# Kernel optimization log

Hardware: AMD Instinct MI355X
Metric: run time of the kernel (lower is better)

## Reference

```python
import jax, jax.numpy as jnp
import numpy as np

H = 16      # num_head
D = 1024    # feat_dim
DK = D // H # per-head dim
B, S = 2, 2048


def setup_inputs() -> dict:
    key = jax.random.key(0)
    ks = jax.random.split(key, 11)
    scale = 1.0 / np.sqrt(D)
    inp = {
        'query': jax.random.normal(ks[0], (B, S, D), jnp.float32),
        'key':   jax.random.normal(ks[1], (B, S, D), jnp.float32),
        'value': jax.random.normal(ks[2], (B, S, D), jnp.float32),
        # causal lower-triangular mask (seq, seq); 0 entries get -1e9
        'mask':  jnp.tril(jnp.ones((S, S), jnp.int32)),
        # torch nn.Linear params: y = x @ W.T + b
        'w_q': jax.random.normal(ks[3], (D, D), jnp.float32) * scale,
        'b_q': jax.random.normal(ks[4], (D,), jnp.float32) * scale,
        'w_k': jax.random.normal(ks[5], (D, D), jnp.float32) * scale,
        'b_k': jax.random.normal(ks[6], (D,), jnp.float32) * scale,
        'w_v': jax.random.normal(ks[7], (D, D), jnp.float32) * scale,
        'b_v': jax.random.normal(ks[8], (D,), jnp.float32) * scale,
        'w_out': jax.random.normal(ks[9], (D, D), jnp.float32) * scale,
        'b_out': jax.random.normal(ks[10], (D,), jnp.float32) * scale,
    }
    return inp


def reference(query, key, value, mask, w_q, b_q, w_k, b_k, w_v, b_v, w_out, b_out):
    b = query.shape[0]
    # projections + split heads -> (b, h, s, d_k)
    def proj(x, w, bias):
        y = x @ w.T + bias
        return y.reshape(b, -1, H, DK).transpose(0, 2, 1, 3)
    q = proj(query, w_q, b_q)
    k = proj(key, w_k, b_k)
    v = proj(value, w_v, b_v)
    # scaled dot-product attention with materialized score matrix
    scores = jnp.einsum('bhqd,bhkd->bhqk', q, k) / np.sqrt(DK).astype(jnp.float32)
    scores = jnp.where(mask == 0, jnp.float32(-1e9), scores)
    attn = jax.nn.softmax(scores, axis=-1)  # dropout is identity in eval mode
    x = jnp.einsum('bhqk,bhkd->bhqd', attn, v)
    x = x.transpose(0, 2, 1, 3).reshape(b, -1, H * DK)
    return x @ w_out.T + b_out
```

## Files before the change

kernel.cpp:

```cpp
#include <hip/hip_runtime.h>

typedef unsigned short u16;
typedef __attribute__((ext_vector_type(8))) short short8;
typedef __attribute__((ext_vector_type(8))) unsigned short u16x8;
typedef __attribute__((ext_vector_type(4))) float floatx4;

#define S2LOG 0.18033688f

__device__ __forceinline__ u16 f2bf(float f) {
    unsigned int u = __float_as_uint(f);
    return (u16)((u + 0x7FFFu + ((u >> 16) & 1u)) >> 16);
}
__device__ __forceinline__ u16 f2bf_hu(float f) {
    return (u16)((__float_as_uint(f) + 0x8000u) >> 16);
}
__device__ __forceinline__ void gl_lds16(const u16* g, u16* l) {
    __builtin_amdgcn_global_load_lds(
        (const __attribute__((address_space(1))) void*)g,
        (__attribute__((address_space(3))) void*)l, 16, 0, 0);
}

__global__ __launch_bounds__(256) void cvt_all(
    const float* __restrict__ q, const float* __restrict__ k, const float* __restrict__ v,
    const float* __restrict__ wq, const float* __restrict__ wk,
    const float* __restrict__ wv, const float* __restrict__ wo,
    u16* __restrict__ ws)
{
    const int b = blockIdx.x, t = threadIdx.x;
    const float* src; u16* dst; long blk;
    if      (b < 2048) { src = q;  dst = ws;            blk = b; }
    else if (b < 4096) { src = k;  dst = ws + 4194304;  blk = b - 2048; }
    else if (b < 6144) { src = v;  dst = ws + 8388608;  blk = b - 4096; }
    else if (b < 6656) { src = wq; dst = ws + 12582912; blk = b - 6144; }
    else if (b < 7168) { src = wk; dst = ws + 13631488; blk = b - 6656; }
    else if (b < 7680) { src = wv; dst = ws + 14680064; blk = b - 7168; }
    else               { src = wo; dst = ws + 15728640; blk = b - 7680; }
    const long i = blk * 2048 + (long)t * 8;
    const float4 a = *(const float4*)(src + i);
    const float4 c = *(const float4*)(src + i + 4);
    u16x8 o;
    o[0] = f2bf(a.x); o[1] = f2bf(a.y); o[2] = f2bf(a.z); o[3] = f2bf(a.w);
    o[4] = f2bf(c.x); o[5] = f2bf(c.y); o[6] = f2bf(c.z); o[7] = f2bf(c.w);
    *(u16x8*)(dst + i) = o;
}

__device__ __forceinline__ void gemm_core64(
    const u16* __restrict__ A, const u16* __restrict__ Bw,
    int m0, int n0, floatx4 (&acc)[2][4])
{
    __shared__ u16 As[128 * 64];
    __shared__ u16 Bs[64 * 64];
    const int t = threadIdx.x, w = t >> 6;
    const int lane = t & 63, col = lane & 15, quad = lane >> 4;
    const int c7 = col & 7;

#pragma unroll
    for (int i = 0; i < 2; ++i)
#pragma unroll
        for (int j = 0; j < 4; ++j) acc[i][j] = (floatx4)0.f;

    for (int k0 = 0; k0 < 1024; k0 += 64) {
#pragma unroll
        for (int jj = 0; jj < 4; ++jj) {
            const int c = jj * 256 + t;
            const int row = c >> 3, kc = (c & 7) ^ (row & 7);
            gl_lds16(A + (size_t)(m0 + row) * 1024 + k0 + kc * 8,
                     As + (jj * 256 + w * 64) * 8);
        }
#pragma unroll
        for (int jj = 0; jj < 2; ++jj) {
            const int c = jj * 256 + t;
            const int row = c >> 3, kc = (c & 7) ^ (row & 7);
            gl_lds16(Bw + (size_t)(n0 + row) * 1024 + k0 + kc * 8,
                     Bs + (jj * 256 + w * 64) * 8);
        }
        __syncthreads();
#pragma unroll
        for (int ks = 0; ks < 2; ++ks) {
            const int swz = (ks * 4 + quad) ^ c7;
            short8 af[2], bf[4];
#pragma unroll
            for (int i = 0; i < 2; ++i)
                af[i] = *(const short8*)&As[((w * 32 + i * 16 + col) * 8 + swz) * 8];
#pragma unroll
            for (int j = 0; j < 4; ++j)
                bf[j] = *(const short8*)&Bs[((j * 16 + col) * 8 + swz) * 8];
#pragma unroll
            for (int i = 0; i < 2; ++i)
#pragma unroll
                for (int j = 0; j < 4; ++j)
                    acc[i][j] = __builtin_amdgcn_mfma_f32_16x16x32_bf16(
                        af[i], bf[j], acc[i][j], 0, 0, 0);
        }
        __syncthreads();
    }
}

__device__ __forceinline__ void gemm_core128(
    const u16* __restrict__ A, const u16* __restrict__ Bw,
    int m0, int n0, floatx4 (&acc)[4][4])
{
    __shared__ u16 As[128 * 64];
    __shared__ u16 Bs[128 * 64];
    const int t = threadIdx.x, w = t >> 6;
    const int lane = t & 63, col = lane & 15, quad = lane >> 4;
    const int c7 = col & 7;
    const int wr = (w >> 1) * 64, wc = (w & 1) * 64;

#pragma unroll
    for (int i = 0; i < 4; ++i)
#pragma unroll
        for (int j = 0; j < 4; ++j) acc[i][j] = (floatx4)0.f;

    for (int k0 = 0; k0 < 1024; k0 += 64) {
#pragma unroll
        for (int jj = 0; jj < 4; ++jj) {
            const int c = jj * 256 + t;
            const int row = c >> 3, kc = (c & 7) ^ (row & 7);
            gl_lds16(A + (size_t)(m0 + row) * 1024 + k0 + kc * 8,
                     As + (jj * 256 + w * 64) * 8);
            gl_lds16(Bw + (size_t)(n0 + row) * 1024 + k0 + kc * 8,
                     Bs + (jj * 256 + w * 64) * 8);
        }
        __syncthreads();
#pragma unroll
        for (int ks = 0; ks < 2; ++ks) {
            const int swz = (ks * 4 + quad) ^ c7;
            short8 af[4], bf[4];
#pragma unroll
            for (int i = 0; i < 4; ++i)
                af[i] = *(const short8*)&As[((wr + i * 16 + col) * 8 + swz) * 8];
#pragma unroll
            for (int j = 0; j < 4; ++j)
                bf[j] = *(const short8*)&Bs[((wc + j * 16 + col) * 8 + swz) * 8];
#pragma unroll
            for (int i = 0; i < 4; ++i)
#pragma unroll
                for (int j = 0; j < 4; ++j)
                    acc[i][j] = __builtin_amdgcn_mfma_f32_16x16x32_bf16(
                        af[i], bf[j], acc[i][j], 0, 0, 0);
        }
        __syncthreads();
    }
}

__global__ __launch_bounds__(256) void gemm_qkv(
    const u16* __restrict__ xq, const u16* __restrict__ xk, const u16* __restrict__ xv,
    const u16* __restrict__ wqb, const u16* __restrict__ wkb, const u16* __restrict__ wvb,
    const float* __restrict__ bq, const float* __restrict__ bk, const float* __restrict__ bv,
    u16* __restrict__ Qh, u16* __restrict__ Kh, u16* __restrict__ Vt)
{
    const int z = blockIdx.z;
    const u16*   A    = z == 0 ? xq  : z == 1 ? xk  : xv;
    const u16*   Bw   = z == 0 ? wqb : z == 1 ? wkb : wvb;
    const float* bias = z == 0 ? bq  : z == 1 ? bk  : bv;
    u16*         out  = z == 0 ? Qh  : z == 1 ? Kh  : Vt;
    const float  scale = z == 0 ? S2LOG : 1.0f;
    const int m0 = blockIdx.x * 128, n0 = blockIdx.y * 128;

    floatx4 acc[4][4];
    gemm_core128(A, Bw, m0, n0, acc);

    const int t = threadIdx.x, w = t >> 6;
    const int lane = t & 63, col = lane & 15, quad = lane >> 4;
    const int wr = (w >> 1) * 64, wc = (w & 1) * 64;
#pragma unroll
    for (int i = 0; i < 4; ++i)
#pragma unroll
        for (int j = 0; j < 4; ++j)
#pragma unroll
            for (int reg = 0; reg < 4; ++reg) {
                const int gm = m0 + wr + i * 16 + quad * 4 + reg;
                const int gn = n0 + wc + j * 16 + col;
                const float val = (acc[i][j][reg] + bias[gn]) * scale;
                const int bb = gm >> 11, ss = gm & 2047, hh = gn >> 6, dd = gn & 63;
                if (z != 2)
                    out[(((size_t)bb * 16 + hh) * 2048 + ss) * 64 + dd] = f2bf(val);
                else
                    out[(((size_t)bb * 16 + hh) * 64 + dd) * 2048 + ss] = f2bf(val);
            }
}

__global__ __launch_bounds__(256) void gemm_out(
    const u16* __restrict__ A, const u16* __restrict__ Bw,
    const float* __restrict__ bias, float* __restrict__ out)
{
    const int m0 = blockIdx.x * 128, n0 = blockIdx.y * 64;
    floatx4 acc[2][4];
    gemm_core64(A, Bw, m0, n0, acc);
    const int t = threadIdx.x, w = t >> 6;
    const int lane = t & 63, col = lane & 15, quad = lane >> 4;
#pragma unroll
    for (int i = 0; i < 2; ++i)
#pragma unroll
        for (int j = 0; j < 4; ++j)
#pragma unroll
            for (int reg = 0; reg < 4; ++reg) {
                const int gm = m0 + w * 32 + i * 16 + quad * 4 + reg;
                const int gn = n0 + j * 16 + col;
                out[(size_t)gm * 1024 + gn] = acc[i][j][reg] + bias[gn];
            }
}

__global__ __launch_bounds__(256) void attn_mfma(
    const u16* __restrict__ Qh, const u16* __restrict__ Kh,
    const u16* __restrict__ Vt, u16* __restrict__ ctx)
{
    __shared__ u16 QPs[128 * 64];
    __shared__ u16 Ks[2][64 * 64];
    __shared__ u16 Vs[2][64 * 64];
    const int t = threadIdx.x, w = t >> 6;
    const int lane = t & 63, col = lane & 15, quad = lane >> 4;
    const int c7 = col & 7;
    const int bh = blockIdx.y;
    const int qt = (bh < 16) ? (15 - (int)blockIdx.x) : (int)blockIdx.x;
    const int q0 = qt * 128;
    const u16* qg = Qh + ((size_t)bh * 2048 + q0) * 64;
    const u16* kg = Kh + (size_t)bh * 2048 * 64;
    const u16* vg = Vt + (size_t)bh * 2048 * 64;

    auto stage = [&](int tile, int buf) {
#pragma unroll
        for (int jj = 0; jj < 2; ++jj) {
            const int c = jj * 256 + t;
            const int row = c >> 3, kc = (c & 7) ^ (row & 7);
            gl_lds16(kg + (size_t)(tile * 64 + row) * 64 + kc * 8,
                     Ks[buf] + (jj * 256 + w * 64) * 8);
            gl_lds16(vg + (size_t)row * 2048 + tile * 64 + kc * 8,
                     Vs[buf] + (jj * 256 + w * 64) * 8);
        }
    };

#pragma unroll
    for (int jj = 0; jj < 4; ++jj) {
        const int c = jj * 256 + t;
        const int row = c >> 3, kc = (c & 7) ^ (row & 7);
        gl_lds16(qg + (size_t)row * 64 + kc * 8, QPs + (jj * 256 + w * 64) * 8);
    }
    stage(0, 0);
    asm volatile("s_waitcnt vmcnt(4)" ::: "memory");
    __builtin_amdgcn_s_barrier();

    short8 qf[2][2];
#pragma unroll
    for (int i = 0; i < 2; ++i)
#pragma unroll
        for (int ks = 0; ks < 2; ++ks)
            qf[i][ks] = *(const short8*)
                &QPs[((w * 32 + i * 16 + col) * 8 + ((ks * 4 + quad) ^ c7)) * 8];
    asm volatile("s_waitcnt lgkmcnt(0)" ::: "memory");
    __builtin_amdgcn_s_barrier();

    floatx4 oacc[2][4], lacc[2];
#pragma unroll
    for (int i = 0; i < 2; ++i) {
        lacc[i] = (floatx4)0.f;
#pragma unroll
        for (int j = 0; j < 4; ++j) oacc[i][j] = (floatx4)0.f;
    }
    short8 ones;
#pragma unroll
    for (int i = 0; i < 8; ++i) ones[i] = (short)0x3F80;

    const int ktmax = 2 * qt + 1;
    int cur = 0;
    for (int kt = 0; kt <= ktmax; ++kt) {
        asm volatile("s_waitcnt vmcnt(0)" ::: "memory");
        __builtin_amdgcn_s_barrier();
        if (kt + 1 <= ktmax) stage(kt + 1, cur ^ 1);

        floatx4 sa[2][4];
#pragma unroll
        for (int i = 0; i < 2; ++i)
#pragma unroll
            for (int j = 0; j < 4; ++j) sa[i][j] = (floatx4)0.f;
#pragma unroll
        for (int ks = 0; ks < 2; ++ks) {
            const int swz = (ks * 4 + quad) ^ c7;
            short8 kf[4];
#pragma unroll
            for (int jc = 0; jc < 4; ++jc)
                kf[jc] = *(const short8*)&Ks[cur][((jc * 16 + col) * 8 + swz) * 8];
#pragma unroll
            for (int i = 0; i < 2; ++i)
#pragma unroll
                for (int jc = 0; jc < 4; ++jc)
                    sa[i][jc] = __builtin_amdgcn_mfma_f32_16x16x32_bf16(
                        qf[i][ks], kf[jc], sa[i][jc], 0, 0, 0);
        }
        const bool pm = (kt >= 2 * qt);
#pragma unroll
        for (int i = 0; i < 2; ++i)
#pragma unroll
            for (int reg = 0; reg < 4; ++reg) {
                const int prow = w * 32 + i * 16 + quad * 4 + reg;
                const int qrow = q0 + prow;
                const int pr7 = (quad * 4 + reg) & 7;
                u16* pr = &QPs[prow * 64 + (col & 7)];
#pragma unroll
                for (int jc = 0; jc < 4; ++jc) {
                    float p = __builtin_amdgcn_exp2f(sa[i][jc][reg]);
                    if (pm && (kt * 64 + jc * 16 + col > qrow)) p = 0.f;
                    pr[((2 * jc + (col >> 3)) ^ pr7) << 3] = f2bf_hu(p);
                }
            }
#pragma unroll
        for (int ks = 0; ks < 2; ++ks) {
            const int swz = (ks * 4 + quad) ^ c7;
            short8 pf[2], vf[4];
#pragma unroll
            for (int i = 0; i < 2; ++i)
                pf[i] = *(const short8*)
                    &QPs[((w * 32 + i * 16 + col) * 8 + swz) * 8];
#pragma unroll
            for (int jd = 0; jd < 4; ++jd)
                vf[jd] = *(const short8*)&Vs[cur][((jd * 16 + col) * 8 + swz) * 8];
#pragma unroll
            for (int i = 0; i < 2; ++i) {
                lacc[i] = __builtin_amdgcn_mfma_f32_16x16x32_bf16(pf[i], ones, lacc[i], 0, 0, 0);
#pragma unroll
                for (int jd = 0; jd < 4; ++jd)
                    oacc[i][jd] = __builtin_amdgcn_mfma_f32_16x16x32_bf16(
                        pf[i], vf[jd], oacc[i][jd], 0, 0, 0);
            }
        }
        cur ^= 1;
    }

    const int bb = bh >> 4, hh = bh & 15;
#pragma unroll
    for (int i = 0; i < 2; ++i)
#pragma unroll
        for (int reg = 0; reg < 4; ++reg) {
            const float inv = __builtin_amdgcn_rcpf(lacc[i][reg]);
            const int qrow = q0 + w * 32 + i * 16 + quad * 4 + reg;
#pragma unroll
            for (int jd = 0; jd < 4; ++jd)
                ctx[((size_t)bb * 2048 + qrow) * 1024 + hh * 64 + jd * 16 + col] =
                    f2bf(oacc[i][jd][reg] * inv);
        }
}

extern "C" void kernel_launch(void* const* d_in, const int* in_sizes, int n_in,
                              void* d_out, int out_size, void* d_ws, size_t ws_size,
                              hipStream_t stream)
{
    const float* query = (const float*)d_in[0];
    const float* key   = (const float*)d_in[1];
    const float* value = (const float*)d_in[2];
    const float* w_q   = (const float*)d_in[4];
    const float* b_q   = (const float*)d_in[5];
    const float* w_k   = (const float*)d_in[6];
    const float* b_k   = (const float*)d_in[7];
    const float* w_v   = (const float*)d_in[8];
    const float* b_v   = (const float*)d_in[9];
    const float* w_out = (const float*)d_in[10];
    const float* b_out = (const float*)d_in[11];

    u16* W = (u16*)d_ws;
    u16* xq  = W;
    u16* xk  = W + 4194304;
    u16* xv  = W + 8388608;
    u16* wqb = W + 12582912;
    u16* wkb = W + 13631488;
    u16* wvb = W + 14680064;
    u16* wob = W + 15728640;
    u16* Qh  = W + 16777216;
    u16* Kh  = W + 20971520;
    u16* Vtw = W + 25165824;
    u16* ctx = W + 29360128;

    hipLaunchKernelGGL(cvt_all, dim3(8192), dim3(256), 0, stream,
                       query, key, value, w_q, w_k, w_v, w_out, W);

    hipLaunchKernelGGL(gemm_qkv, dim3(32, 8, 3), dim3(256), 0, stream,
                       xq, xk, xv, wqb, wkb, wvb, b_q, b_k, b_v, Qh, Kh, Vtw);

    hipLaunchKernelGGL(attn_mfma, dim3(16, 32), dim3(256), 0, stream, Qh, Kh, Vtw, ctx);

    hipLaunchKernelGGL(gemm_out, dim3(32, 16), dim3(256), 0, stream,
                       ctx, wob, b_out, (float*)d_out);
}
```

Baseline: 248.2 us.

## Double-buffer LDS tiles in projection GEMMs to overlap loads with MFMA

Both GEMM cores now keep two LDS buffers for the A and B tiles. The next K-slice is issued via global_load_lds right after the barrier, while MFMAs run on the current buffer. One barrier per iteration replaces two, and explicit waitcnts guard the buffers. LDS use doubles (up to 64KB in the 128 core), which can lower occupancy. Correctness relies on the vmcnt wait plus barrier ordering being enough for the asynchronous LDS writes.

```diff
diff --git a/kernel.cpp b/kernel.cpp
--- a/kernel.cpp
+++ b/kernel.cpp
@@ -48,8 +48,8 @@
     const u16* __restrict__ A, const u16* __restrict__ Bw,
     int m0, int n0, floatx4 (&acc)[2][4])
 {
-    __shared__ u16 As[128 * 64];
-    __shared__ u16 Bs[64 * 64];
+    __shared__ u16 As[2][128 * 64];
+    __shared__ u16 Bs[2][64 * 64];
     const int t = threadIdx.x, w = t >> 6;
     const int lane = t & 63, col = lane & 15, quad = lane >> 4;
     const int c7 = col & 7;
@@ -59,32 +59,39 @@
 #pragma unroll
         for (int j = 0; j < 4; ++j) acc[i][j] = (floatx4)0.f;
 
-    for (int k0 = 0; k0 < 1024; k0 += 64) {
+    auto stage = [&](int k0, int buf) {
 #pragma unroll
         for (int jj = 0; jj < 4; ++jj) {
             const int c = jj * 256 + t;
             const int row = c >> 3, kc = (c & 7) ^ (row & 7);
             gl_lds16(A + (size_t)(m0 + row) * 1024 + k0 + kc * 8,
-                     As + (jj * 256 + w * 64) * 8);
+                     As[buf] + (jj * 256 + w * 64) * 8);
         }
 #pragma unroll
         for (int jj = 0; jj < 2; ++jj) {
             const int c = jj * 256 + t;
             const int row = c >> 3, kc = (c & 7) ^ (row & 7);
             gl_lds16(Bw + (size_t)(n0 + row) * 1024 + k0 + kc * 8,
-                     Bs + (jj * 256 + w * 64) * 8);
-        }
-        __syncthreads();
+                     Bs[buf] + (jj * 256 + w * 64) * 8);
+        }
+    };
+
+    stage(0, 0);
+    int cur = 0;
+    for (int k0 = 0; k0 < 1024; k0 += 64) {
+        asm volatile("s_waitcnt vmcnt(0)" ::: "memory");
+        __builtin_amdgcn_s_barrier();
+        if (k0 + 64 < 1024) stage(k0 + 64, cur ^ 1);
 #pragma unroll
         for (int ks = 0; ks < 2; ++ks) {
             const int swz = (ks * 4 + quad) ^ c7;
             short8 af[2], bf[4];
 #pragma unroll
             for (int i = 0; i < 2; ++i)
-                af[i] = *(const short8*)&As[((w * 32 + i * 16 + col) * 8 + swz) * 8];
+                af[i] = *(const short8*)&As[cur][((w * 32 + i * 16 + col) * 8 + swz) * 8];
 #pragma unroll
             for (int j = 0; j < 4; ++j)
-                bf[j] = *(const short8*)&Bs[((j * 16 + col) * 8 + swz) * 8];
+                bf[j] = *(const short8*)&Bs[cur][((j * 16 + col) * 8 + swz) * 8];
 #pragma unroll
             for (int i = 0; i < 2; ++i)
 #pragma unroll
@@ -92,7 +99,8 @@
                     acc[i][j] = __builtin_amdgcn_mfma_f32_16x16x32_bf16(
                         af[i], bf[j], acc[i][j], 0, 0, 0);
         }
-        __syncthreads();
+        asm volatile("s_waitcnt lgkmcnt(0)" ::: "memory");
+        cur ^= 1;
     }
 }
 
@@ -100,8 +108,8 @@
     const u16* __restrict__ A, const u16* __restrict__ Bw,
     int m0, int n0, floatx4 (&acc)[4][4])
 {
-    __shared__ u16 As[128 * 64];
-    __shared__ u16 Bs[128 * 64];
+    __shared__ u16 As[2][128 * 64];
+    __shared__ u16 Bs[2][128 * 64];
     const int t = threadIdx.x, w = t >> 6;
     const int lane = t & 63, col = lane & 15, quad = lane >> 4;
     const int c7 = col & 7;
@@ -112,27 +120,34 @@
 #pragma unroll
         for (int j = 0; j < 4; ++j) acc[i][j] = (floatx4)0.f;
 
-    for (int k0 = 0; k0 < 1024; k0 += 64) {
+    auto stage = [&](int k0, int buf) {
 #pragma unroll
         for (int jj = 0; jj < 4; ++jj) {
             const int c = jj * 256 + t;
             const int row = c >> 3, kc = (c & 7) ^ (row & 7);
             gl_lds16(A + (size_t)(m0 + row) * 1024 + k0 + kc * 8,
-                     As + (jj * 256 + w * 64) * 8);
+                     As[buf] + (jj * 256 + w * 64) * 8);
             gl_lds16(Bw + (size_t)(n0 + row) * 1024 + k0 + kc * 8,
-                     Bs + (jj * 256 + w * 64) * 8);
-        }
-        __syncthreads();
+                     Bs[buf] + (jj * 256 + w * 64) * 8);
+        }
+    };
+
+    stage(0, 0);
+    int cur = 0;
+    for (int k0 = 0; k0 < 1024; k0 += 64) {
+        asm volatile("s_waitcnt vmcnt(0)" ::: "memory");
+        __builtin_amdgcn_s_barrier();
+        if (k0 + 64 < 1024) stage(k0 + 64, cur ^ 1);
 #pragma unroll
         for (int ks = 0; ks < 2; ++ks) {
             const int swz = (ks * 4 + quad) ^ c7;
             short8 af[4], bf[4];
 #pragma unroll
             for (int i = 0; i < 4; ++i)
-                af[i] = *(const short8*)&As[((wr + i * 16 + col) * 8 + swz) * 8];
+                af[i] = *(const short8*)&As[cur][((wr + i * 16 + col) * 8 + swz) * 8];
 #pragma unroll
             for (int j = 0; j < 4; ++j)
-                bf[j] = *(const short8*)&Bs[((wc + j * 16 + col) * 8 + swz) * 8];
+                bf[j] = *(const short8*)&Bs[cur][((wc + j * 16 + col) * 8 + swz) * 8];
 #pragma unroll
             for (int i = 0; i < 4; ++i)
 #pragma unroll
@@ -140,7 +155,8 @@
                     acc[i][j] = __builtin_amdgcn_mfma_f32_16x16x32_bf16(
                         af[i], bf[j], acc[i][j], 0, 0, 0);
         }
-        __syncthreads();
+        asm volatile("s_waitcnt lgkmcnt(0)" ::: "memory");
+        cur ^= 1;
     }
 }
 
```

Result: no change. 244.9 us (-1.3%).
